# Optimization experiments

Measured on AMD Instinct MI355X. Metric: run time of the kernel, lower is better.

## Reference

```python
import jax, jax.numpy as jnp
import numpy as np

N_NODES = 50000
NEG_SLOPE = 0.2  # PyG GATConv default
EPS = 1e-16      # PyG softmax denominator epsilon


def _gat_conv(x, edge_index, W, att_src, att_dst, bias):
    """Single-head PyG-style GATConv with self-loops.
    x: [N, F_in], edge_index: [2, E] (row 0 = src/j, row 1 = dst/i).
    """
    n = x.shape[0]
    loop = jnp.arange(n, dtype=edge_index.dtype)
    src = jnp.concatenate([edge_index[0], loop])  # [E+N]
    dst = jnp.concatenate([edge_index[1], loop])  # [E+N]

    h = x @ W                                      # [N, F_out]
    a_src = h @ att_src                            # [N]
    a_dst = h @ att_dst                            # [N]

    e = jax.nn.leaky_relu(a_src[src] + a_dst[dst], NEG_SLOPE)  # [E+N]
    # segment softmax over incoming edges of each dst node
    m = jax.ops.segment_max(e, dst, num_segments=n)
    m = jnp.where(jnp.isfinite(m), m, 0.0)
    e = jnp.exp(e - m[dst])
    s = jax.ops.segment_sum(e, dst, num_segments=n)
    alpha = e / (s[dst] + EPS)                     # [E+N]

    out = jax.ops.segment_sum(alpha[:, None] * h[src], dst, num_segments=n)
    return out + bias


def setup_inputs() -> dict:
    key = jax.random.key(0)
    ks = jax.random.split(key, 10)
    d_in, d_hid, d_emb = 128, 64, 64
    n_edges = 800000
    x = jax.random.normal(ks[0], (N_NODES, d_in), dtype=jnp.float32)
    edge_index = jax.random.randint(ks[1], (2, n_edges), 0, N_NODES, dtype=jnp.int64)
    def glorot(k, shape):
        lim = float(np.sqrt(6.0 / sum(shape)))
        return jax.random.uniform(k, shape, jnp.float32, -lim, lim)
    return {
        "x": x,
        "edge_index": edge_index,
        "W1": glorot(ks[2], (d_in, d_hid)),
        "att_src1": glorot(ks[3], (d_hid,)),
        "att_dst1": glorot(ks[4], (d_hid,)),
        "b1": jnp.zeros((d_hid,), jnp.float32),
        "W2": glorot(ks[5], (d_hid, d_emb)),
        "att_src2": glorot(ks[6], (d_emb,)),
        "att_dst2": glorot(ks[7], (d_emb,)),
        "b2": jnp.zeros((d_emb,), jnp.float32),
    }


def reference(x, edge_index, W1, att_src1, att_dst1, b1, W2, att_src2, att_dst2, b2):
    x1 = jax.nn.relu(_gat_conv(x, edge_index, W1, att_src1, att_dst1, b1))
    # dropout is identity in eval mode
    x2 = _gat_conv(x1, edge_index, W2, att_src2, att_dst2, b2)
    return x2
```

## Files before the change

kernel.cpp:

```cpp
#include <hip/hip_runtime.h>
#include <hip/hip_bf16.h>

#define F_OUT 64
#define NEG_SLOPE 0.2f
#define SOFT_EPS 1e-16f
#define BW 256
#define CH 8192
#define TH 512

typedef short short8 __attribute__((ext_vector_type(8)));
typedef float floatx4 __attribute__((ext_vector_type(4)));
typedef unsigned short ushort4v __attribute__((ext_vector_type(4)));

__device__ __forceinline__ unsigned short f2bf_bits(float v) {
    __hip_bfloat16 hb = __float2bfloat16(v);
    return *(unsigned short*)&hb;
}
__device__ __forceinline__ float bf_bits2f(unsigned short u) {
    __hip_bfloat16 hb = *(__hip_bfloat16*)&u;
    return __bfloat162float(hb);
}
__device__ __forceinline__ float read_any(const void* src, int off, int bf) {
    return bf ? __bfloat162float(((const __hip_bfloat16*)src)[off])
              : ((const float*)src)[off];
}
__device__ __forceinline__ int get_idx(const void* ei, int i64, long long pos) {
    return i64 ? (int)((const long long*)ei)[pos] : ((const int*)ei)[pos];
}

__device__ __forceinline__ void detect_local(const unsigned* wbits, const unsigned* ebits,
                                             int* sm_bf, int* sm_i64) {
    if (threadIdx.x < 64) {
        unsigned w = wbits[threadIdx.x];
        unsigned e = (w >> 7) & 0xFFu;
        unsigned long long mb = __ballot(e >= 0x60u && e <= 0x7Eu);
        unsigned long long mz = __ballot(ebits[2 * threadIdx.x + 1] == 0u);
        if (threadIdx.x == 0) { *sm_bf = (__popcll(mb) > 32); *sm_i64 = (__popcll(mz) > 32); }
    }
    __syncthreads();
}

__global__ void count_prep(const void* __restrict__ ei, int* __restrict__ table,
                           const void* w1, const void* as1, const void* ad1, const void* b1,
                           const void* w2, const void* as2, const void* ad2, const void* b2,
                           unsigned short* __restrict__ wt1, unsigned short* __restrict__ wt2,
                           float* __restrict__ vecs, int* __restrict__ flags,
                           int E, int total, int NB, int nchunks, int n1, int n2, int K1) {
    __shared__ int cnt[1024];
    __shared__ int s_bf, s_i64;
    detect_local((const unsigned*)w1, (const unsigned*)ei, &s_bf, &s_i64);
    int bf = s_bf, i64 = s_i64;
    int g = blockIdx.x, tid = threadIdx.x;
    if (g == 0 && tid == 0) { flags[0] = bf; flags[1] = i64; }

    if (g < nchunks) {
        for (int k = tid; k < NB; k += TH) cnt[k] = 0;
        __syncthreads();
        int base = g * CH;
        int lim = base + CH < total ? base + CH : total;
        for (int t = base + tid; t < lim; t += TH) {
            int i = t < E ? get_idx(ei, i64, (long long)E + t) : t - E;
            atomicAdd(&cnt[i >> 8], 1);
        }
        __syncthreads();
        for (int k = tid; k < NB; k += TH) table[k * nchunks + g] = cnt[k];
    } else {
        int wtotal = n1 + n2 + 384;
        for (int t = tid; t < wtotal; t += TH) {
            if (t < n1) {
                int n = t / K1, k = t - n * K1;
                wt1[t] = f2bf_bits(read_any(w1, k * F_OUT + n, bf));
            } else if (t < n1 + n2) {
                int u = t - n1;
                int n = u >> 6, k = u & 63;
                wt2[u] = f2bf_bits(read_any(w2, k * F_OUT + n, bf));
            } else {
                int u = t - n1 - n2;
                const void* srcp[6] = {as1, ad1, b1, as2, ad2, b2};
                vecs[u] = read_any(srcp[u >> 6], u & 63, bf);
            }
        }
    }
}

template <int K>
__device__ __forceinline__ void gemm_body(int blk, int tid,
                          const void* __restrict__ xv, const unsigned short* __restrict__ Wt,
                          const float* __restrict__ att_s, const float* __restrict__ att_d,
                          unsigned short* __restrict__ h, float* __restrict__ a_s,
                          float* __restrict__ a_d, int N, int bf) {
    int lane = tid & 63;
    int m0 = (blk * 4 + (tid >> 6)) * 16;
    if (m0 >= N) return;
    int c = lane & 15, quad = lane >> 4;
    int arow = m0 + c;
    if (arow >= N) arow = N - 1;

    floatx4 acc0 = {0.f, 0.f, 0.f, 0.f};
    floatx4 acc1 = acc0, acc2 = acc0, acc3 = acc0;

    for (int kc = 0; kc < K; kc += 32) {
        int ka = kc + quad * 8;
        short8 a;
        if (bf) {
            a = *(const short8*)((const unsigned short*)xv + (size_t)arow * K + ka);
        } else {
            const float* xp = (const float*)xv + (size_t)arow * K + ka;
#pragma unroll
            for (int j = 0; j < 8; ++j) a[j] = (short)f2bf_bits(xp[j]);
        }
        short8 b0 = *(const short8*)(Wt + (size_t)(c)      * K + ka);
        short8 b1 = *(const short8*)(Wt + (size_t)(16 + c) * K + ka);
        short8 b2 = *(const short8*)(Wt + (size_t)(32 + c) * K + ka);
        short8 b3 = *(const short8*)(Wt + (size_t)(48 + c) * K + ka);
        acc0 = __builtin_amdgcn_mfma_f32_16x16x32_bf16(a, b0, acc0, 0, 0, 0);
        acc1 = __builtin_amdgcn_mfma_f32_16x16x32_bf16(a, b1, acc1, 0, 0, 0);
        acc2 = __builtin_amdgcn_mfma_f32_16x16x32_bf16(a, b2, acc2, 0, 0, 0);
        acc3 = __builtin_amdgcn_mfma_f32_16x16x32_bf16(a, b3, acc3, 0, 0, 0);
    }

    float as0 = att_s[c],      as1 = att_s[16 + c], as2 = att_s[32 + c], as3 = att_s[48 + c];
    float ad0 = att_d[c],      ad1 = att_d[16 + c], ad2 = att_d[32 + c], ad3 = att_d[48 + c];
#pragma unroll
    for (int reg = 0; reg < 4; ++reg) {
        int row = m0 + quad * 4 + reg;
        float vs = acc0[reg] * as0 + acc1[reg] * as1 + acc2[reg] * as2 + acc3[reg] * as3;
        float vd = acc0[reg] * ad0 + acc1[reg] * ad1 + acc2[reg] * ad2 + acc3[reg] * ad3;
#pragma unroll
        for (int off = 1; off < 16; off <<= 1) {
            vs += __shfl_xor(vs, off);
            vd += __shfl_xor(vd, off);
        }
        if (row < N) {
            if (c == 0) { a_s[row] = vs; a_d[row] = vd; }
            unsigned short* hr = h + (size_t)row * F_OUT + c;
            hr[0]  = f2bf_bits(acc0[reg]);
            hr[16] = f2bf_bits(acc1[reg]);
            hr[32] = f2bf_bits(acc2[reg]);
            hr[48] = f2bf_bits(acc3[reg]);
        }
    }
}

__global__ void gemm1_scanA(const void* __restrict__ xv, const unsigned short* __restrict__ Wt,
                            const float* __restrict__ att_s, const float* __restrict__ att_d,
                            unsigned short* __restrict__ h, float* __restrict__ a_s,
                            float* __restrict__ a_d, int N, const int* __restrict__ flags,
                            const int* __restrict__ table, int* __restrict__ bsum,
                            int M, int blkGemm) {
    if ((int)blockIdx.x < blkGemm) {
        gemm_body<128>(blockIdx.x, threadIdx.x, xv, Wt, att_s, att_d, h, a_s, a_d, N, flags[0]);
        return;
    }
    int bid = blockIdx.x - blkGemm;
    int idx = bid * 1024 + threadIdx.x * 4;
    int s = 0;
#pragma unroll
    for (int j = 0; j < 4; ++j) { int k = idx + j; if (k < M) s += table[k]; }
#pragma unroll
    for (int off = 1; off < 64; off <<= 1) s += __shfl_xor(s, off);
    __shared__ int ws[4];
    int lane = threadIdx.x & 63, w = threadIdx.x >> 6;
    if (lane == 0) ws[w] = s;
    __syncthreads();
    if (threadIdx.x == 0) bsum[bid] = ws[0] + ws[1] + ws[2] + ws[3];
}

__global__ void scanC(int* __restrict__ data, const int* __restrict__ bsum, int n, int nbM,
                      int* __restrict__ extra, int extra_val) {
    __shared__ int sb[64];
    int tid = threadIdx.x;
    if (tid < 64) sb[tid] = (tid < nbM) ? bsum[tid] : 0;
    __syncthreads();
    int carry = 0;
    for (int k = 0; k < (int)blockIdx.x; ++k) carry += sb[k];
    if (blockIdx.x == 0 && tid == 0 && extra) *extra = extra_val;

    int idx = blockIdx.x * 1024 + tid * 4;
    int lane = tid & 63, w = tid >> 6;
    int d[4];
#pragma unroll
    for (int j = 0; j < 4; ++j) d[j] = (idx + j < n) ? data[idx + j] : 0;
    int tot = d[0] + d[1] + d[2] + d[3];
    int v = tot;
#pragma unroll
    for (int off = 1; off < 64; off <<= 1) {
        int t = __shfl_up(v, off);
        if (lane >= off) v += t;
    }
    __shared__ int wtot[4];
    if (lane == 63) wtot[w] = v;
    __syncthreads();
    int woff = 0;
    for (int k = 0; k < w; ++k) woff += wtot[k];
    int excl = v - tot + woff + carry;
    int o[4];
    o[0] = excl; o[1] = o[0] + d[0]; o[2] = o[1] + d[1]; o[3] = o[2] + d[2];
#pragma unroll
    for (int j = 0; j < 4; ++j)
        if (idx + j < n) data[idx + j] = o[j];
}

__global__ void stage_scatter(const void* __restrict__ ei, const int* __restrict__ table,
                              unsigned* __restrict__ staged, const unsigned* __restrict__ wbits,
                              int E, int total, int NB, int nchunks) {
    __shared__ int cur[1024];
    __shared__ int s_bf, s_i64;
    detect_local(wbits, (const unsigned*)ei, &s_bf, &s_i64);
    int i64 = s_i64;
    for (int k = threadIdx.x; k < NB; k += TH) cur[k] = table[k * nchunks + blockIdx.x];
    __syncthreads();
    int base = blockIdx.x * CH;
    int lim = base + CH < total ? base + CH : total;
    for (int t = base + threadIdx.x; t < lim; t += TH) {
        int i = t < E ? get_idx(ei, i64, (long long)E + t) : t - E;
        int j = t < E ? get_idx(ei, i64, t) : t - E;
        int pos = atomicAdd(&cur[i >> 8], 1);
        staged[pos] = ((unsigned)(i & 255) << 24) | (unsigned)j;
    }
}

__global__ void bucket_csr(const unsigned* __restrict__ staged, const int* __restrict__ table,
                           int* __restrict__ row_ptr, int* __restrict__ eidx,
                           int N, int total, int NB, int nchunks) {
    __shared__ int ldeg[BW];
    __shared__ int lcur[BW];
    __shared__ int wtot[4];
    int b = blockIdx.x;
    int t = threadIdx.x;
    int seg_beg = table[b * nchunks];
    int seg_end = (b + 1 < NB) ? table[(b + 1) * nchunks] : total;
    ldeg[t] = 0;
    __syncthreads();
    for (int p = seg_beg + t; p < seg_end; p += 256)
        atomicAdd(&ldeg[staged[p] >> 24], 1);
    __syncthreads();
    int lane = t & 63, w = t >> 6;
    int d = ldeg[t];
    int v = d;
#pragma unroll
    for (int off = 1; off < 64; off <<= 1) {
        int u = __shfl_up(v, off);
        if (lane >= off) v += u;
    }
    if (lane == 63) wtot[w] = v;
    __syncthreads();
    int woff = 0;
    for (int k = 0; k < w; ++k) woff += wtot[k];
    int excl = v - d + woff;
    int node = b * BW + t;
    if (node < N) row_ptr[node] = seg_beg + excl;
    lcur[t] = excl;
    __syncthreads();
    for (int p = seg_beg + t; p < seg_end; p += 256) {
        unsigned pk = staged[p];
        int pos = atomicAdd(&lcur[pk >> 24], 1);
        eidx[seg_beg + pos] = (int)(pk & 0xFFFFFFu);
    }
}

__global__ void mfma_gemm2(const void* __restrict__ xv, const unsigned short* __restrict__ Wt,
                           const float* __restrict__ att_s, const float* __restrict__ att_d,
                           unsigned short* __restrict__ h, float* __restrict__ a_s,
                           float* __restrict__ a_d, int N) {
    gemm_body<64>(blockIdx.x, threadIdx.x, xv, Wt, att_s, att_d, h, a_s, a_d, N, 1);
}

__global__ void node_gather(const int* __restrict__ row_ptr, const int* __restrict__ eidx,
                            const float* __restrict__ a_s, const float* __restrict__ a_d,
                            const unsigned short* __restrict__ h, const float* __restrict__ bias,
                            void* __restrict__ out, int N,
                            const int* __restrict__ flags, int mode) {
    int lane = threadIdx.x & 63;
    int i = blockIdx.x * 4 + (threadIdx.x >> 6);
    if (i >= N) return;
    int quad = lane >> 4, c = lane & 15;
    int beg = row_ptr[i];
    int end = row_ptr[i + 1];
    float ad = a_d[i];
    float se = 0.f;
    floatx4 acc[4];
#pragma unroll
    for (int k = 0; k < 4; ++k) acc[k] = (floatx4){0.f, 0.f, 0.f, 0.f};

    for (int p = beg; p < end; p += 64) {
        int tile = end - p; if (tile > 64) tile = 64;
        int jm = eidx[p + (lane < tile ? lane : tile - 1)];
        float wm = 0.f;
        if (lane < tile) {
            float e = a_s[jm] + ad;
            wm = __expf(e > 0.f ? e : NEG_SLOPE * e);
        }
        se += wm;
        for (int e = 0; e < tile; e += 16) {
#pragma unroll
            for (int k = 0; k < 4; ++k) {
                if (e + 4 * k < tile) {
                    int idx = e + 4 * k + quad;
                    int srcl = idx < tile ? idx : tile - 1;
                    int jk = __shfl(jm, srcl);
                    float wk = __shfl(wm, srcl);
                    if (idx >= tile) wk = 0.f;
                    ushort4v hv = *(const ushort4v*)(h + (size_t)jk * F_OUT + (c << 2));
                    acc[k][0] += wk * bf_bits2f(hv[0]);
                    acc[k][1] += wk * bf_bits2f(hv[1]);
                    acc[k][2] += wk * bf_bits2f(hv[2]);
                    acc[k][3] += wk * bf_bits2f(hv[3]);
                }
            }
        }
    }
#pragma unroll
    for (int off = 1; off < 64; off <<= 1) se += __shfl_xor(se, off);
    floatx4 A = (acc[0] + acc[1]) + (acc[2] + acc[3]);
#pragma unroll
    for (int m = 0; m < 4; ++m) {
        A[m] += __shfl_xor(A[m], 16);
        A[m] += __shfl_xor(A[m], 32);
    }
    if (quad == 0) {
        int col = c << 2;
        float inv = 1.f / (se + SOFT_EPS);
        float v0 = A[0] * inv + bias[col];
        float v1 = A[1] * inv + bias[col + 1];
        float v2 = A[2] * inv + bias[col + 2];
        float v3 = A[3] * inv + bias[col + 3];
        size_t o = (size_t)i * F_OUT + col;
        if (mode == 0) {
            ushort4v ov;
            ov[0] = f2bf_bits(v0 > 0.f ? v0 : 0.f);
            ov[1] = f2bf_bits(v1 > 0.f ? v1 : 0.f);
            ov[2] = f2bf_bits(v2 > 0.f ? v2 : 0.f);
            ov[3] = f2bf_bits(v3 > 0.f ? v3 : 0.f);
            *(ushort4v*)((unsigned short*)out + o) = ov;
        } else if (flags[0]) {
            ushort4v ov;
            ov[0] = f2bf_bits(v0); ov[1] = f2bf_bits(v1);
            ov[2] = f2bf_bits(v2); ov[3] = f2bf_bits(v3);
            *(ushort4v*)((unsigned short*)out + o) = ov;
        } else {
            floatx4 ov = {v0, v1, v2, v3};
            *(floatx4*)((float*)out + o) = ov;
        }
    }
}

extern "C" void kernel_launch(void* const* d_in, const int* in_sizes, int n_in,
                              void* d_out, int out_size, void* d_ws, size_t ws_size,
                              hipStream_t stream) {
    const void* x   = d_in[0];
    const void* ei  = d_in[1];
    const void* W1  = d_in[2];
    const void* as1 = d_in[3];
    const void* ad1 = d_in[4];
    const void* b1  = d_in[5];
    const void* W2  = d_in[6];
    const void* as2 = d_in[7];
    const void* ad2 = d_in[8];
    const void* b2  = d_in[9];

    int E  = in_sizes[1] / 2;
    int n1 = in_sizes[2];
    int n2 = in_sizes[6];
    int K1 = n1 / F_OUT;
    int N  = in_sizes[0] / K1;
    int total = E + N;
    int NB = (N + BW - 1) / BW;
    int nchunks = (total + CH - 1) / CH;
    int M = NB * nchunks;
    int nbM = (M + 1023) / 1024;

    size_t nf = (size_t)N * F_OUT;
    char* wsb = (char*)d_ws;
    unsigned short* h   = (unsigned short*)wsb;
    unsigned short* x1b = h + nf;
    unsigned short* wt1 = x1b + nf;
    unsigned short* wt2 = wt1 + n1;
    float* a_s  = (float*)(wt2 + n2 + ((n1 + n2) & 1));
    float* a_d  = a_s + N;
    float* vecs = a_d + N;
    float* cAs1 = vecs,       *cAd1 = vecs + 64,  *cB1 = vecs + 128;
    float* cAs2 = vecs + 192, *cAd2 = vecs + 256, *cB2 = vecs + 320;
    int* flags    = (int*)(vecs + 384);
    int* row_ptr  = flags + 8;
    int* eidx     = row_ptr + N + 1;
    unsigned* staged = (unsigned*)(eidx + total);
    int* table    = (int*)(staged + total);
    int* bsum     = table + M;

    int blkGemm = (N + 63) / 64;
    int blkNode = (N + 3) / 4;

    count_prep<<<nchunks + 1, TH, 0, stream>>>(ei, table, W1, as1, ad1, b1,
                                               W2, as2, ad2, b2, wt1, wt2, vecs, flags,
                                               E, total, NB, nchunks, n1, n2, K1);
    gemm1_scanA<<<blkGemm + nbM, 256, 0, stream>>>(x, wt1, cAs1, cAd1, h, a_s, a_d, N,
                                                   flags, table, bsum, M, blkGemm);
    scanC<<<nbM, 256, 0, stream>>>(table, bsum, M, nbM, row_ptr + N, total);
    stage_scatter<<<nchunks, TH, 0, stream>>>(ei, table, staged, (const unsigned*)W1,
                                              E, total, NB, nchunks);
    bucket_csr<<<NB, 256, 0, stream>>>(staged, table, row_ptr, eidx, N, total, NB, nchunks);
    node_gather<<<blkNode, 256, 0, stream>>>(row_ptr, eidx, a_s, a_d, h, cB1, x1b, N, flags, 0);
    mfma_gemm2<<<blkGemm, 256, 0, stream>>>(x1b, wt2, cAs2, cAd2, h, a_s, a_d, N);
    node_gather<<<blkNode, 256, 0, stream>>>(row_ptr, eidx, a_s, a_d, h, cB2, d_out, N, flags, 1);
}
```

Measured before the change: 213.0 us.

## Fuse bucket-offset scan into scatter kernel and co-schedule GEMM1 with it

Removes the separate two-kernel scan of the bucket/chunk count table. Each scatter block now recomputes its own bucket offsets by reading every row of the table and running a block-wide prefix scan in shared memory. The first-layer GEMM blocks (now 8 waves per block) ride in the same launch as the scatter blocks. This cuts two kernel launches and their dependencies, but every scatter block redundantly reads the full table and does a serial scan with many __syncthreads, and the GEMM now uses a different wave grouping.

Result: faster. 207.1 us (-2.8%).

```diff
diff --git a/kernel.cpp b/kernel.cpp
--- a/kernel.cpp
+++ b/kernel.cpp
@@ -83,14 +83,14 @@
     }
 }
 
-template <int K>
+template <int K, int WAVES>
 __device__ __forceinline__ void gemm_body(int blk, int tid,
                           const void* __restrict__ xv, const unsigned short* __restrict__ Wt,
                           const float* __restrict__ att_s, const float* __restrict__ att_d,
                           unsigned short* __restrict__ h, float* __restrict__ a_s,
                           float* __restrict__ a_d, int N, int bf) {
     int lane = tid & 63;
-    int m0 = (blk * 4 + (tid >> 6)) * 16;
+    int m0 = (blk * WAVES + (tid >> 6)) * 16;
     if (m0 >= N) return;
     int c = lane & 15, quad = lane >> 4;
     int arow = m0 + c;
@@ -142,94 +142,73 @@
     }
 }
 
-__global__ void gemm1_scanA(const void* __restrict__ xv, const unsigned short* __restrict__ Wt,
-                            const float* __restrict__ att_s, const float* __restrict__ att_d,
-                            unsigned short* __restrict__ h, float* __restrict__ a_s,
-                            float* __restrict__ a_d, int N, const int* __restrict__ flags,
-                            const int* __restrict__ table, int* __restrict__ bsum,
-                            int M, int blkGemm) {
-    if ((int)blockIdx.x < blkGemm) {
-        gemm_body<128>(blockIdx.x, threadIdx.x, xv, Wt, att_s, att_d, h, a_s, a_d, N, flags[0]);
-        return;
-    }
-    int bid = blockIdx.x - blkGemm;
-    int idx = bid * 1024 + threadIdx.x * 4;
-    int s = 0;
-#pragma unroll
-    for (int j = 0; j < 4; ++j) { int k = idx + j; if (k < M) s += table[k]; }
-#pragma unroll
-    for (int off = 1; off < 64; off <<= 1) s += __shfl_xor(s, off);
-    __shared__ int ws[4];
-    int lane = threadIdx.x & 63, w = threadIdx.x >> 6;
-    if (lane == 0) ws[w] = s;
-    __syncthreads();
-    if (threadIdx.x == 0) bsum[bid] = ws[0] + ws[1] + ws[2] + ws[3];
-}
-
-__global__ void scanC(int* __restrict__ data, const int* __restrict__ bsum, int n, int nbM,
-                      int* __restrict__ extra, int extra_val) {
-    __shared__ int sb[64];
-    int tid = threadIdx.x;
-    if (tid < 64) sb[tid] = (tid < nbM) ? bsum[tid] : 0;
-    __syncthreads();
-    int carry = 0;
-    for (int k = 0; k < (int)blockIdx.x; ++k) carry += sb[k];
-    if (blockIdx.x == 0 && tid == 0 && extra) *extra = extra_val;
-
-    int idx = blockIdx.x * 1024 + tid * 4;
-    int lane = tid & 63, w = tid >> 6;
-    int d[4];
-#pragma unroll
-    for (int j = 0; j < 4; ++j) d[j] = (idx + j < n) ? data[idx + j] : 0;
-    int tot = d[0] + d[1] + d[2] + d[3];
-    int v = tot;
-#pragma unroll
-    for (int off = 1; off < 64; off <<= 1) {
-        int t = __shfl_up(v, off);
-        if (lane >= off) v += t;
-    }
-    __shared__ int wtot[4];
-    if (lane == 63) wtot[w] = v;
-    __syncthreads();
-    int woff = 0;
-    for (int k = 0; k < w; ++k) woff += wtot[k];
-    int excl = v - tot + woff + carry;
-    int o[4];
-    o[0] = excl; o[1] = o[0] + d[0]; o[2] = o[1] + d[1]; o[3] = o[2] + d[2];
-#pragma unroll
-    for (int j = 0; j < 4; ++j)
-        if (idx + j < n) data[idx + j] = o[j];
-}
-
-__global__ void stage_scatter(const void* __restrict__ ei, const int* __restrict__ table,
-                              unsigned* __restrict__ staged, const unsigned* __restrict__ wbits,
-                              int E, int total, int NB, int nchunks) {
-    __shared__ int cur[1024];
+__global__ void __launch_bounds__(TH)
+scatter_gemm1(const void* __restrict__ ei, const int* __restrict__ table,
+              unsigned* __restrict__ staged, int* __restrict__ segbeg,
+              int* __restrict__ row_ptr, const void* __restrict__ xv,
+              const unsigned short* __restrict__ Wt,
+              const float* __restrict__ att_s, const float* __restrict__ att_d,
+              unsigned short* __restrict__ h, float* __restrict__ a_s,
+              float* __restrict__ a_d, const unsigned* __restrict__ wbits,
+              int E, int total, int NB, int nchunks, int N) {
     __shared__ int s_bf, s_i64;
     detect_local(wbits, (const unsigned*)ei, &s_bf, &s_i64);
+    int tid = threadIdx.x;
+    if ((int)blockIdx.x >= nchunks) {
+        gemm_body<128, 8>(blockIdx.x - nchunks, tid, xv, Wt, att_s, att_d,
+                          h, a_s, a_d, N, s_bf);
+        return;
+    }
+    __shared__ int s_scan[TH];
+    __shared__ int s_cur[1024];
+    int g = blockIdx.x;
     int i64 = s_i64;
-    for (int k = threadIdx.x; k < NB; k += TH) cur[k] = table[k * nchunks + blockIdx.x];
-    __syncthreads();
-    int base = blockIdx.x * CH;
+    int b0 = 0;
+    if (tid < NB) {
+        const int* row = table + (size_t)tid * nchunks;
+        int rsum = 0, rpart = 0;
+        for (int c2 = 0; c2 < nchunks; ++c2) {
+            int v = row[c2];
+            rsum += v;
+            rpart += (c2 < g) ? v : 0;
+        }
+        b0 = rsum;
+        s_cur[tid] = rpart;
+    }
+    s_scan[tid] = (tid < NB) ? b0 : 0;
+    __syncthreads();
+    for (int off = 1; off < TH; off <<= 1) {
+        int v = (tid >= off) ? s_scan[tid - off] : 0;
+        __syncthreads();
+        s_scan[tid] += v;
+        __syncthreads();
+    }
+    if (tid < NB) {
+        int excl = s_scan[tid] - b0;
+        s_cur[tid] = excl + s_cur[tid];
+        if (g == 0) segbeg[tid] = excl;
+    }
+    if (g == 0 && tid == 0) { segbeg[NB] = total; row_ptr[N] = total; }
+    __syncthreads();
+    int base = g * CH;
     int lim = base + CH < total ? base + CH : total;
-    for (int t = base + threadIdx.x; t < lim; t += TH) {
+    for (int t = base + tid; t < lim; t += TH) {
         int i = t < E ? get_idx(ei, i64, (long long)E + t) : t - E;
         int j = t < E ? get_idx(ei, i64, t) : t - E;
-        int pos = atomicAdd(&cur[i >> 8], 1);
+        int pos = atomicAdd(&s_cur[i >> 8], 1);
         staged[pos] = ((unsigned)(i & 255) << 24) | (unsigned)j;
     }
 }
 
-__global__ void bucket_csr(const unsigned* __restrict__ staged, const int* __restrict__ table,
-                           int* __restrict__ row_ptr, int* __restrict__ eidx,
-                           int N, int total, int NB, int nchunks) {
+__global__ void bucket_csr(const unsigned* __restrict__ staged, const int* __restrict__ segbeg,
+                           int* __restrict__ row_ptr, int* __restrict__ eidx, int N) {
     __shared__ int ldeg[BW];
     __shared__ int lcur[BW];
     __shared__ int wtot[4];
     int b = blockIdx.x;
     int t = threadIdx.x;
-    int seg_beg = table[b * nchunks];
-    int seg_end = (b + 1 < NB) ? table[(b + 1) * nchunks] : total;
+    int seg_beg = segbeg[b];
+    int seg_end = segbeg[b + 1];
     ldeg[t] = 0;
     __syncthreads();
     for (int p = seg_beg + t; p < seg_end; p += 256)
@@ -263,7 +242,7 @@
                            const float* __restrict__ att_s, const float* __restrict__ att_d,
                            unsigned short* __restrict__ h, float* __restrict__ a_s,
                            float* __restrict__ a_d, int N) {
-    gemm_body<64>(blockIdx.x, threadIdx.x, xv, Wt, att_s, att_d, h, a_s, a_d, N, 1);
+    gemm_body<64, 4>(blockIdx.x, threadIdx.x, xv, Wt, att_s, att_d, h, a_s, a_d, N, 1);
 }
 
 __global__ void node_gather(const int* __restrict__ row_ptr, const int* __restrict__ eidx,
@@ -368,7 +347,6 @@
     int NB = (N + BW - 1) / BW;
     int nchunks = (total + CH - 1) / CH;
     int M = NB * nchunks;
-    int nbM = (M + 1023) / 1024;
 
     size_t nf = (size_t)N * F_OUT;
     char* wsb = (char*)d_ws;
@@ -386,21 +364,21 @@
     int* eidx     = row_ptr + N + 1;
     unsigned* staged = (unsigned*)(eidx + total);
     int* table    = (int*)(staged + total);
-    int* bsum     = table + M;
-
-    int blkGemm = (N + 63) / 64;
+    int* segbeg   = table + M;
+
+    int blkG1 = (N + 127) / 128;
+    int blkG2 = (N + 63) / 64;
     int blkNode = (N + 3) / 4;
 
     count_prep<<<nchunks + 1, TH, 0, stream>>>(ei, table, W1, as1, ad1, b1,
                                                W2, as2, ad2, b2, wt1, wt2, vecs, flags,
                                                E, total, NB, nchunks, n1, n2, K1);
-    gemm1_scanA<<<blkGemm + nbM, 256, 0, stream>>>(x, wt1, cAs1, cAd1, h, a_s, a_d, N,
-                                                   flags, table, bsum, M, blkGemm);
-    scanC<<<nbM, 256, 0, stream>>>(table, bsum, M, nbM, row_ptr + N, total);
-    stage_scatter<<<nchunks, TH, 0, stream>>>(ei, table, staged, (const unsigned*)W1,
-                                              E, total, NB, nchunks);
-    bucket_csr<<<NB, 256, 0, stream>>>(staged, table, row_ptr, eidx, N, total, NB, nchunks);
+    scatter_gemm1<<<nchunks + blkG1, TH, 0, stream>>>(ei, table, staged, segbeg, row_ptr,
+                                                      x, wt1, cAs1, cAd1, h, a_s, a_d,
+                                                      (const unsigned*)W1,
+                                                      E, total, NB, nchunks, N);
+    bucket_csr<<<NB, 256, 0, stream>>>(staged, segbeg, row_ptr, eidx, N);
     node_gather<<<blkNode, 256, 0, stream>>>(row_ptr, eidx, a_s, a_d, h, cB1, x1b, N, flags, 0);
-    mfma_gemm2<<<blkGemm, 256, 0, stream>>>(x1b, wt2, cAs2, cAd2, h, a_s, a_d, N);
+    mfma_gemm2<<<blkG2, 256, 0, stream>>>(x1b, wt2, cAs2, cAd2, h, a_s, a_d, N);
     node_gather<<<blkNode, 256, 0, stream>>>(row_ptr, eidx, a_s, a_d, h, cB2, d_out, N, flags, 1);
 }
```
